# Kernel optimization log

Measured on AMD Instinct MI355X. Metric: run time of the kernel, lower is better.

The kernel has to match this reference:

```python
import jax, jax.numpy as jnp
import numpy as np

N = 2048
TEMP = 1.0


def _conv(x, w, b):
    y = jax.lax.conv_general_dilated(x, w, (1, 1), 'VALID',
                                     dimension_numbers=('NCHW', 'OIHW', 'NCHW'))
    return y + b[None, :, None, None]


def _pool(x):
    return jax.lax.reduce_window(x, -jnp.inf, jax.lax.max,
                                 (1, 1, 2, 2), (1, 1, 2, 2), 'VALID')


def setup_inputs() -> dict:
    key = jax.random.key(0)
    ks = jax.random.split(key, 20)
    s = 0.05
    idx = jnp.arange(N)
    positions = jnp.stack([idx // 64, idx % 64], axis=1).astype(jnp.int32)  # 32x64 grid
    return {
        'x': jax.random.normal(ks[0], (1, N, 1, 32, 32), jnp.float32),
        'positions': positions,
        'conv1_w': jax.random.normal(ks[1], (36, 1, 4, 4), jnp.float32) * s,
        'conv1_b': jnp.zeros((36,), jnp.float32),
        'conv2_w': jax.random.normal(ks[2], (48, 36, 3, 3), jnp.float32) * s,
        'conv2_b': jnp.zeros((48,), jnp.float32),
        'fc1_w': jax.random.normal(ks[3], (512, 1728), jnp.float32) * s,
        'fc1_b': jnp.zeros((512,), jnp.float32),
        'fc2_w': jax.random.normal(ks[4], (512, 512), jnp.float32) * s,
        'fc2_b': jnp.zeros((512,), jnp.float32),
        'nbr_w': jax.random.normal(ks[5], (512, 512), jnp.float32) * s,
        'nbr_b': jnp.zeros((512,), jnp.float32),
        'templates': jax.random.normal(ks[6], (10, 1024), jnp.float32),
        'proto_w': jax.random.normal(ks[7], (1024, 1024), jnp.float32) * s,
        'proto_b': jnp.zeros((1024,), jnp.float32),
        'glob_w1': jax.random.normal(ks[8], (128, 1024), jnp.float32) * s,
        'glob_b1': jnp.zeros((128,), jnp.float32),
        'glob_w2': jax.random.normal(ks[9], (1, 128), jnp.float32) * s,
        'glob_b2': jnp.zeros((1,), jnp.float32),
        'cls_w': jax.random.normal(ks[10], (2, 1024), jnp.float32) * s,
        'cls_b': jnp.zeros((2,), jnp.float32),
    }


def reference(x, positions, conv1_w, conv1_b, conv2_w, conv2_b,
              fc1_w, fc1_b, fc2_w, fc2_b, nbr_w, nbr_b,
              templates, proto_w, proto_b, glob_w1, glob_b1,
              glob_w2, glob_b2, cls_w, cls_b):
    xs = x[0]                                    # squeeze bag dim -> [N,1,32,32]
    h = _pool(jax.nn.relu(_conv(xs, conv1_w, conv1_b)))
    h = _pool(jax.nn.relu(_conv(h, conv2_w, conv2_b)))
    H = h.reshape(h.shape[0], -1)                # [N,1728]
    H = jax.nn.relu(H @ fc1_w.T + fc1_b)         # dropout is identity in eval
    H = jax.nn.relu(H @ fc2_w.T + fc2_b)         # [N,512]

    # --- neighbourhood attention (vectorized GAT-style gather/softmax) ---
    d = jnp.max(jnp.abs(positions[:, None, :] - positions[None, :, :]), axis=-1)
    mask = (d > 0) & (d <= 1)                    # [N,N] neighbor mask
    has = mask.any(axis=1)
    mask = jnp.where(has[:, None], mask, jnp.eye(mask.shape[0], dtype=bool))  # fallback: self
    An = jnp.tanh(H @ nbr_w.T + nbr_b)           # [N,512]
    logits = H @ An.T                            # logits[i,j] = tanh(W h_j) . h_i
    alphas = jax.nn.softmax(jnp.where(mask, logits, -jnp.inf), axis=1)
    Hn = alphas @ H                              # neighbourhood embeddings [N,512]
    H2 = jnp.concatenate([H, Hn], axis=1)        # [N,1024]

    # --- template (prototype) attention ---
    betas = jax.nn.softmax((jnp.tanh(H2 @ proto_w.T + proto_b) @ templates.T).T / TEMP, axis=1)  # [T,N]
    embs = betas @ H2                            # [T,1024]

    # --- global attention over templates ---
    g = jnp.tanh(embs @ glob_w1.T + glob_b1) @ glob_w2.T + glob_b2  # [T,1]
    gammas = jax.nn.softmax(g.T / TEMP, axis=1)  # [1,T]
    M = gammas @ embs                            # [1,1024]
    A = gammas @ betas                           # [1,N]
    Y_prob = jax.nn.sigmoid(M @ cls_w.T + cls_b) # [1,2]
    Y_hat = jnp.argmax(Y_prob, axis=1)
    return Y_prob, Y_hat, A
```

## Files before the change

kernel.cpp:

```cpp
#include <hip/hip_runtime.h>
#include <hip/hip_bf16.h>
#include <math.h>


typedef short short8 __attribute__((ext_vector_type(8)));
typedef float f32x4  __attribute__((ext_vector_type(4)));

__device__ inline short f2bf(float f) {
    unsigned u = __builtin_bit_cast(unsigned, f);
    u += 0x7fff + ((u >> 16) & 1);
    return (short)(u >> 16);
}
__device__ inline float bf2f(short h) {
    unsigned u = ((unsigned)(unsigned short)h) << 16;
    return __builtin_bit_cast(float, u);
}
__device__ inline f32x4 mfma16(short8 a, short8 b, f32x4 c) {
    return __builtin_amdgcn_mfma_f32_16x16x32_bf16(a, b, c, 0, 0, 0);
}
__device__ inline void splitstore(const float* s, short* hi, short* lo, int i) {
    float f = s[i];
    short h = f2bf(f);
    hi[i] = h;
    lo[i] = f2bf(f - bf2f(h));
}

__global__ __launch_bounds__(256) void prep_all_kernel(
    const float* __restrict__ fc1w, short* __restrict__ fc1whi, short* __restrict__ fc1wlo,
    const float* __restrict__ fc2w, short* __restrict__ fc2whi, short* __restrict__ fc2wlo,
    const float* __restrict__ nbrw, short* __restrict__ nbrwhi, short* __restrict__ nbrwlo,
    const float* __restrict__ prw,  short* __restrict__ prwhi,  short* __restrict__ prwlo,
    const float* __restrict__ w1,   short* __restrict__ w1m,
    const float* __restrict__ w2,   short* __restrict__ w2m,
    float* __restrict__ St, float* __restrict__ embs)
{
    const int b = blockIdx.x, tid = threadIdx.x;
    if (b < 3456) {
        int i = b*256 + tid; if (i < 884736) splitstore(fc1w, fc1whi, fc1wlo, i);
    } else if (b < 4480) {
        int i = (b-3456)*256 + tid; if (i < 262144) splitstore(fc2w, fc2whi, fc2wlo, i);
    } else if (b < 5504) {
        int i = (b-4480)*256 + tid; if (i < 262144) splitstore(nbrw, nbrwhi, nbrwlo, i);
    } else if (b < 9600) {
        int i = (b-5504)*256 + tid; if (i < 1048576) splitstore(prw, prwhi, prwlo, i);
    } else if (b < 9606) {
        int i = (b-9600)*256 + tid;
        if (i < 1536) {
            int c = i >> 5, k = i & 31;
            w1m[i] = (c < 36 && k < 16) ? f2bf(w1[c*16 + k]) : (short)0;
        }
    } else if (b < 9714) {
        int i = (b-9606)*256 + tid;
        if (i < 27648) {
            int oc = i / 576, r = i % 576, tap = r >> 6, c = r & 63;
            w2m[i] = (c < 36) ? f2bf(w2[oc*324 + c*9 + tap]) : (short)0;
        }
    } else if (b < 9794) {
        int i = (b-9714)*256 + tid; if (i < 20480) St[i] = 0.0f;
    } else {
        int i = (b-9794)*256 + tid; if (i < 10240) embs[i] = 0.0f;
    }
}

__global__ __launch_bounds__(64, 2) void conv_mfma_kernel(
    const float* __restrict__ x,
    const short* __restrict__ w1m,
    const float* __restrict__ b1,
    const short* __restrict__ w2m,
    const float* __restrict__ b2,
    short* __restrict__ Hfhi)
{
    __shared__ __align__(16) short sxb[2][1024];
    __shared__ __align__(16) short sh1[196*40 + 32];
    const int n = blockIdx.x, l = threadIdx.x;
    const int g = l >> 4, fr = l & 15;

    #pragma unroll
    for (int i = 0; i < 4; ++i) {
        const float4 v4 = ((const float4*)(x + (size_t)n*1024))[l + 64*i];
        short v[4] = { f2bf(v4.x), f2bf(v4.y), f2bf(v4.z), f2bf(v4.w) };
        const int c4 = (l + 64*i)*4;
        *(short4*)&sxb[0][c4] = *(short4*)v;
        if (c4 & 31) sxb[1][c4-1] = v[0];
        sxb[1][c4+0] = v[1];
        sxb[1][c4+1] = v[2];
        sxb[1][c4+2] = v[3];
    }
    if (l < 4) { short8 z = {}; *(short8*)&sh1[196*40 + l*8] = z; }
    short8 bw1[3];
    #pragma unroll
    for (int nt = 0; nt < 3; ++nt)
        bw1[nt] = *(const short8*)(w1m + (nt*16 + fr)*32 + g*8);
    __syncthreads();

    for (int mt = 0; mt < 49; ++mt) {
        const int pp = mt*16 + fr;
        const int q = pp >> 2, dd = pp & 3;
        const int iy0 = 2*(q/14) + (dd >> 1), ix0 = 2*(q%14) + (dd & 1);
        short8 af = {};
        if (g < 2) {
            const int par = ix0 & 1;
            const int colp = ix0 - par;
            const unsigned* p0 = (const unsigned*)&sxb[par][(iy0 + 2*g)*32 + colp];
            union { unsigned u[4]; short8 s; } uu;
            uu.u[0] = p0[0];  uu.u[1] = p0[1];
            uu.u[2] = p0[16]; uu.u[3] = p0[17];
            af = uu.s;
        }
        f32x4 acc[3] = {};
        #pragma unroll
        for (int nt = 0; nt < 3; ++nt) acc[nt] = mfma16(af, bw1[nt], acc[nt]);
        const int q1 = mt*4 + g;
        #pragma unroll
        for (int nt = 0; nt < 3; ++nt) {
            const int c = nt*16 + fr;
            if (c < 36) {
                float m = fmaxf(fmaxf(acc[nt][0], acc[nt][1]),
                                fmaxf(acc[nt][2], acc[nt][3]));
                m = fmaxf(m + b1[c], 0.0f);
                *(short*)((char*)sh1 + (q1*80 + c*2)) = f2bf(m);
            } else if (c < 40) {
                *(short*)((char*)sh1 + (q1*80 + c*2)) = 0;
            }
        }
    }
    __syncthreads();

    #pragma unroll
    for (int nt = 0; nt < 3; ++nt) {
        short8 bfr[18];
        {
            const short* wb = w2m + (size_t)(nt*16 + fr)*576 + g*8;
            #pragma unroll
            for (int ks = 0; ks < 18; ++ks)
                bfr[ks] = *(const short8*)(wb + ks*32);
        }
        for (int mt = 0; mt < 9; ++mt) {
            const int pp = mt*16 + fr;
            const int q2 = pp >> 2, dd = pp & 3;
            const int oy = 2*(q2/6) + (dd >> 1), ox = 2*(q2%6) + (dd & 1);
            f32x4 acc = {};
            #pragma unroll
            for (int ks = 0; ks < 18; ++ks) {
                const int tap = ks >> 1, half = ks & 1;
                const int hr = (oy + tap/3)*14 + ox + tap%3;
                const short8 a = *(const short8*)((char*)sh1 +
                    (hr*80 + half*64 + g*16));
                acc = mfma16(a, bfr[ks], acc);
            }
            const int oc = nt*16 + fr;
            float m = fmaxf(fmaxf(acc[0], acc[1]), fmaxf(acc[2], acc[3]));
            m = fmaxf(m + b2[oc], 0.0f);
            Hfhi[(size_t)n*1728 + oc*36 + (mt*4 + g)] = f2bf(m);
        }
    }
}

template<int ACT, int OUTF32, int OUTBF, int TSC>
__global__ __launch_bounds__(512, 2) void gemm_split_kernel(
    const short* __restrict__ Ahi,
    const short* __restrict__ Whi, const short* __restrict__ Wlo,
    const float* __restrict__ bias,
    float* __restrict__ Cf, short* __restrict__ Chi,
    const float* __restrict__ Tm, float* __restrict__ St,
    const int N, const int K)
{
    __shared__ __align__(16) short sA[4096];
    __shared__ __align__(16) short sB[2][4096];
    const int bn = blockIdx.x, bm = blockIdx.y;
    const int tid = threadIdx.x, l = tid & 63, w = tid >> 6, g = l >> 4, fr = l & 15;
    const int wm = w & 3, wn = w >> 2;
    const int srow = tid >> 3;
    const int wbyte = srow*128 + (tid & 7)*16;
    const int swb = (srow & 7) << 4;
    const size_t aoff = (size_t)(bm*64 + srow)*K + (tid & 7)*8;
    const size_t boff = (size_t)(bn*64 + srow)*K + (tid & 7)*8;
    f32x4 acc[2] = {};
    short8 ra = *(const short8*)(Ahi + aoff);
    short8 rb0 = *(const short8*)(Whi + boff);
    short8 rb1 = *(const short8*)(Wlo + boff);
    for (int k0 = 0; k0 < K; k0 += 64) {
        __syncthreads();
        *(short8*)((char*)sA       + (wbyte ^ swb)) = ra;
        *(short8*)((char*)&sB[0][0] + (wbyte ^ swb)) = rb0;
        *(short8*)((char*)&sB[1][0] + (wbyte ^ swb)) = rb1;
        __syncthreads();
        if (k0 + 64 < K) {
            ra  = *(const short8*)(Ahi + aoff + k0 + 64);
            rb0 = *(const short8*)(Whi + boff + k0 + 64);
            rb1 = *(const short8*)(Wlo + boff + k0 + 64);
        }
        const int ar = wm*16 + fr, asw = (ar & 7) << 4;
        const short8 ah0 = *(const short8*)((char*)sA + ((ar*128      + g*16) ^ asw));
        const short8 ah1 = *(const short8*)((char*)sA + ((ar*128 + 64 + g*16) ^ asw));
        #pragma unroll
        for (int ntl = 0; ntl < 2; ++ntl) {
            const int br = (wn*2 + ntl)*16 + fr, bsw = (br & 7) << 4;
            const short8 bh0 = *(const short8*)((char*)&sB[0][0] + ((br*128      + g*16) ^ bsw));
            const short8 bh1 = *(const short8*)((char*)&sB[0][0] + ((br*128 + 64 + g*16) ^ bsw));
            const short8 bl0 = *(const short8*)((char*)&sB[1][0] + ((br*128      + g*16) ^ bsw));
            const short8 bl1 = *(const short8*)((char*)&sB[1][0] + ((br*128 + 64 + g*16) ^ bsw));
            acc[ntl] = mfma16(ah0, bh0, acc[ntl]);
            acc[ntl] = mfma16(ah1, bh1, acc[ntl]);
            acc[ntl] = mfma16(ah0, bl0, acc[ntl]);
            acc[ntl] = mfma16(ah1, bl1, acc[ntl]);
        }
    }
    float pv[2][4];
    #pragma unroll
    for (int ntl = 0; ntl < 2; ++ntl) {
        const int col = bn*64 + (wn*2 + ntl)*16 + fr;
        const float bv = bias[col];
        #pragma unroll
        for (int i = 0; i < 4; ++i) {
            const int row = bm*64 + wm*16 + g*4 + i;
            float v = acc[ntl][i] + bv;
            if (ACT == 1) v = fmaxf(v, 0.0f);
            if (ACT == 2) v = tanhf(v);
            pv[ntl][i] = v;
            const size_t idx = (size_t)row*N + col;
            if (OUTF32) Cf[idx] = v;
            if (OUTBF)  Chi[idx] = f2bf(v);
        }
    }
    if (TSC) {
        for (int t = 0; t < 10; ++t) {
            float tm[2];
            #pragma unroll
            for (int ntl = 0; ntl < 2; ++ntl)
                tm[ntl] = Tm[t*1024 + bn*64 + (wn*2 + ntl)*16 + fr];
            float part[4];
            #pragma unroll
            for (int i = 0; i < 4; ++i) {
                float s = 0.0f;
                #pragma unroll
                for (int ntl = 0; ntl < 2; ++ntl) s = fmaf(pv[ntl][i], tm[ntl], s);
                #pragma unroll
                for (int m = 1; m <= 8; m <<= 1) s += __shfl_xor(s, m);
                part[i] = s;
            }
            if (fr == 0) {
                #pragma unroll
                for (int i = 0; i < 4; ++i)
                    atomicAdd(&St[t*2048 + bm*64 + wm*16 + g*4 + i], part[i]);
            }
        }
    }
}

__global__ __launch_bounds__(64) void nbr_attn_kernel(
    const float* __restrict__ H, const float* __restrict__ An,
    short* __restrict__ H2hi)
{
    const int i = blockIdx.x;
    const int lane = threadIdx.x;
    const int r = i >> 6, c = i & 63;
    const int DR[8] = {-1,-1,-1, 0, 0, 1, 1, 1};
    const int DC[8] = {-1, 0, 1,-1, 1,-1, 0, 1};
    int nbr[8]; bool val[8];
    #pragma unroll
    for (int j = 0; j < 8; ++j) {
        const int rr = r + DR[j], cc = c + DC[j];
        val[j] = (rr >= 0 && rr < 32 && cc >= 0 && cc < 64);
        nbr[j] = val[j] ? rr*64 + cc : i;
    }
    float hi[8];
    #pragma unroll
    for (int q = 0; q < 8; ++q) hi[q] = H[(size_t)i*512 + q*64 + lane];
    float av[8][8];
    #pragma unroll
    for (int j = 0; j < 8; ++j) {
        const float* an = An + (size_t)nbr[j]*512 + lane;
        #pragma unroll
        for (int q = 0; q < 8; ++q) av[j][q] = an[q*64];
    }
    float lg[8];
    #pragma unroll
    for (int j = 0; j < 8; ++j) {
        float s = 0.0f;
        #pragma unroll
        for (int q = 0; q < 8; ++q) s = fmaf(hi[q], av[j][q], s);
        #pragma unroll
        for (int off = 32; off; off >>= 1) s += __shfl_xor(s, off);
        lg[j] = val[j] ? s : -1e30f;
    }
    float mx = -1e30f;
    #pragma unroll
    for (int j = 0; j < 8; ++j) mx = fmaxf(mx, lg[j]);
    float sum = 0.0f; float al[8];
    #pragma unroll
    for (int j = 0; j < 8; ++j) { al[j] = expf(lg[j]-mx); sum += al[j]; }
    const float inv = 1.0f/sum;
    #pragma unroll
    for (int j = 0; j < 8; ++j) {
        const float* hj = H + (size_t)nbr[j]*512 + lane;
        #pragma unroll
        for (int q = 0; q < 8; ++q) av[j][q] = hj[q*64];
    }
    float hn[8] = {};
    #pragma unroll
    for (int j = 0; j < 8; ++j) {
        const float a = al[j]*inv;
        #pragma unroll
        for (int q = 0; q < 8; ++q) hn[q] = fmaf(a, av[j][q], hn[q]);
    }
    #pragma unroll
    for (int q = 0; q < 8; ++q) {
        const size_t i0 = (size_t)i*1024 + q*64 + lane;
        H2hi[i0]       = f2bf(hi[q]);
        H2hi[i0 + 512] = f2bf(hn[q]);
    }
}

__global__ __launch_bounds__(256) void beta_embs_kernel(
    const float* __restrict__ St,
    const short* __restrict__ H2hi,
    float* __restrict__ embs,
    float* __restrict__ minv)
{
    const int t = blockIdx.y;
    const int tid = threadIdx.x;
    __shared__ float red[256];
    __shared__ float sb[256];
    float mx = -1e30f;
    for (int n = tid; n < 2048; n += 256) mx = fmaxf(mx, St[t*2048+n]);
    red[tid] = mx; __syncthreads();
    for (int s = 128; s; s >>= 1) { if (tid < s) red[tid] = fmaxf(red[tid], red[tid+s]); __syncthreads(); }
    mx = red[0]; __syncthreads();
    float sum = 0.0f;
    for (int n = tid; n < 2048; n += 256) sum += expf(St[t*2048+n]-mx);
    red[tid] = sum; __syncthreads();
    for (int s = 128; s; s >>= 1) { if (tid < s) red[tid] += red[tid+s]; __syncthreads(); }
    const float inv = 1.0f/red[0];
    if (blockIdx.x == 0 && tid == 0) { minv[t*2+0] = mx; minv[t*2+1] = inv; }
    const int colc = blockIdx.x & 3;
    const int nc   = blockIdx.x >> 2;
    sb[tid] = expf(St[t*2048 + nc*256 + tid] - mx) * inv;
    __syncthreads();
    const int col = colc*256 + tid;
    float acc = 0.0f;
    for (int j = 0; j < 256; ++j)
        acc = fmaf(sb[j], bf2f(H2hi[(size_t)(nc*256+j)*1024 + col]), acc);
    atomicAdd(&embs[t*1024+col], acc);
}

__global__ __launch_bounds__(64) void glob_g2_kernel(
    const float* __restrict__ embs, const float* __restrict__ gw1,
    const float* __restrict__ gb1, const float* __restrict__ gw2,
    float* __restrict__ gpart)
{
    const int k = blockIdx.x, t = blockIdx.y, lane = threadIdx.x;
    const float* e  = embs + t*1024 + lane;
    const float* wv = gw1 + k*1024 + lane;
    float s = 0.0f;
    #pragma unroll
    for (int q = 0; q < 16; ++q) s = fmaf(e[q*64], wv[q*64], s);
    #pragma unroll
    for (int off = 32; off; off >>= 1) s += __shfl_xor(s, off);
    if (lane == 0) gpart[t*128 + k] = tanhf(s + gb1[k]) * gw2[k];
}

__global__ __launch_bounds__(256) void final3_kernel(
    const float* __restrict__ gpart, const float* __restrict__ gb2,
    const float* __restrict__ embs,  const float* __restrict__ St,
    const float* __restrict__ minv,
    const float* __restrict__ cw, const float* __restrict__ cb,
    float* __restrict__ out)
{
    __shared__ float gam[10];
    __shared__ float sM[1024];
    __shared__ float red[256];
    __shared__ float gv[10];
    __shared__ float smx[10], sinv[10];
    __shared__ float v0s;
    const int tid = threadIdx.x;
    for (int t = 0; t < 10; ++t) {
        float s = (tid < 128) ? gpart[t*128 + tid] : 0.0f;
        red[tid] = s; __syncthreads();
        for (int st = 128; st; st >>= 1) { if (tid < st) red[tid] += red[tid+st]; __syncthreads(); }
        if (tid == 0) gv[t] = red[0];
        __syncthreads();
    }
    if (tid < 10) { smx[tid] = minv[tid*2]; sinv[tid] = minv[tid*2+1]; }
    if (tid == 0) {
        float mx = -1e30f;
        for (int t = 0; t < 10; ++t) mx = fmaxf(mx, gv[t] + gb2[0]);
        float sum = 0.0f;
        for (int t = 0; t < 10; ++t) { gam[t] = expf(gv[t] + gb2[0] - mx); sum += gam[t]; }
        for (int t = 0; t < 10; ++t) gam[t] /= sum;
    }
    __syncthreads();
    for (int col = tid; col < 1024; col += 256) {
        float m = 0.0f;
        for (int t = 0; t < 10; ++t) m = fmaf(gam[t], embs[t*1024+col], m);
        sM[col] = m;
    }
    for (int n = tid; n < 2048; n += 256) {
        float a = 0.0f;
        for (int t = 0; t < 10; ++t)
            a = fmaf(gam[t], expf(St[t*2048+n]-smx[t])*sinv[t], a);
        out[3+n] = a;
    }
    __syncthreads();
    float s0 = 0.0f, s1 = 0.0f;
    for (int q = tid; q < 1024; q += 256) {
        s0 = fmaf(sM[q], cw[q], s0);
        s1 = fmaf(sM[q], cw[1024+q], s1);
    }
    red[tid] = s0; __syncthreads();
    for (int s = 128; s; s >>= 1) { if (tid < s) red[tid] += red[tid+s]; __syncthreads(); }
    if (tid == 0) v0s = red[0];
    __syncthreads();
    red[tid] = s1; __syncthreads();
    for (int s = 128; s; s >>= 1) { if (tid < s) red[tid] += red[tid+s]; __syncthreads(); }
    if (tid == 0) {
        const float l0 = v0s + cb[0], l1 = red[0] + cb[1];
        const float p0 = 1.0f/(1.0f+expf(-l0));
        const float p1 = 1.0f/(1.0f+expf(-l1));
        out[0] = p0; out[1] = p1;
        out[2] = (p1 > p0) ? 1.0f : 0.0f;
    }
}

extern "C" void kernel_launch(void* const* d_in, const int* in_sizes, int n_in,
                              void* d_out, int out_size, void* d_ws, size_t ws_size,
                              hipStream_t stream)
{
    (void)in_sizes; (void)n_in; (void)out_size; (void)ws_size;
    const float* x        = (const float*)d_in[0];
    const float* conv1_w  = (const float*)d_in[2];
    const float* conv1_b  = (const float*)d_in[3];
    const float* conv2_w  = (const float*)d_in[4];
    const float* conv2_b  = (const float*)d_in[5];
    const float* fc1_w    = (const float*)d_in[6];
    const float* fc1_b    = (const float*)d_in[7];
    const float* fc2_w    = (const float*)d_in[8];
    const float* fc2_b    = (const float*)d_in[9];
    const float* nbr_w    = (const float*)d_in[10];
    const float* nbr_b    = (const float*)d_in[11];
    const float* templ    = (const float*)d_in[12];
    const float* proto_w  = (const float*)d_in[13];
    const float* proto_b  = (const float*)d_in[14];
    const float* glob_w1  = (const float*)d_in[15];
    const float* glob_b1  = (const float*)d_in[16];
    const float* glob_w2  = (const float*)d_in[17];
    const float* glob_b2  = (const float*)d_in[18];
    const float* cls_w    = (const float*)d_in[19];
    const float* cls_b    = (const float*)d_in[20];
    float* out = (float*)d_out;

    char* p = (char*)d_ws;
    auto alloc = [&](size_t bytes) { char* r = p; p += (bytes + 255) & ~(size_t)255; return r; };
    short* Hfhi   = (short*)alloc((size_t)2048*1728*2);
    short* Hfc1hi = (short*)alloc((size_t)2048*512*2);
    float* H      = (float*)alloc((size_t)2048*512*4);
    short* Hhi    = (short*)alloc((size_t)2048*512*2);
    float* An     = (float*)alloc((size_t)2048*512*4);
    short* H2hi   = (short*)alloc((size_t)2048*1024*2);
    float* St     = (float*)alloc((size_t)10*2048*4);
    float* minv   = (float*)alloc(10*2*4);
    float* embs   = (float*)alloc((size_t)10*1024*4);
    float* gpart  = (float*)alloc((size_t)10*128*4);
    short* w1m    = (short*)alloc(1536*2);
    short* w2m    = (short*)alloc(27648*2);
    short* fc1whi = (short*)alloc((size_t)512*1728*2);
    short* fc1wlo = (short*)alloc((size_t)512*1728*2);
    short* fc2whi = (short*)alloc((size_t)512*512*2);
    short* fc2wlo = (short*)alloc((size_t)512*512*2);
    short* nbrwhi = (short*)alloc((size_t)512*512*2);
    short* nbrwlo = (short*)alloc((size_t)512*512*2);
    short* prwhi  = (short*)alloc((size_t)1024*1024*2);
    short* prwlo  = (short*)alloc((size_t)1024*1024*2);

    prep_all_kernel<<<9834, 256, 0, stream>>>(
        fc1_w, fc1whi, fc1wlo, fc2_w, fc2whi, fc2wlo,
        nbr_w, nbrwhi, nbrwlo, proto_w, prwhi, prwlo,
        conv1_w, w1m, conv2_w, w2m, St, embs);

    conv_mfma_kernel<<<2048, 64, 0, stream>>>(x, w1m, conv1_b, w2m, conv2_b, Hfhi);
    gemm_split_kernel<1,0,1,0><<<dim3(8,32), 512, 0, stream>>>(
        Hfhi, fc1whi, fc1wlo, fc1_b, nullptr, Hfc1hi, nullptr, nullptr, 512, 1728);
    gemm_split_kernel<1,1,1,0><<<dim3(8,32), 512, 0, stream>>>(
        Hfc1hi, fc2whi, fc2wlo, fc2_b, H, Hhi, nullptr, nullptr, 512, 512);
    gemm_split_kernel<2,1,0,0><<<dim3(8,32), 512, 0, stream>>>(
        Hhi, nbrwhi, nbrwlo, nbr_b, An, nullptr, nullptr, nullptr, 512, 512);
    nbr_attn_kernel<<<2048, 64, 0, stream>>>(H, An, H2hi);
    gemm_split_kernel<2,0,0,1><<<dim3(16,32), 512, 0, stream>>>(
        H2hi, prwhi, prwlo, proto_b, nullptr, nullptr, templ, St, 1024, 1024);
    beta_embs_kernel<<<dim3(32,10), 256, 0, stream>>>(St, H2hi, embs, minv);
    glob_g2_kernel<<<dim3(128,10), 64, 0, stream>>>(embs, glob_w1, glob_b1, glob_w2, gpart);
    final3_kernel<<<1, 256, 0, stream>>>(gpart, glob_b2, embs, St, minv, cls_w, cls_b, out);
}
```

Before: 161.5 us.

## Pack conv2 weights to drop channel padding and reuse A fragments across output tiles

Conv2's im2col K dimension drops from 18 padded k-steps (64 channels per tap, 36 real) to 11 packed k-steps. The leftover 4 channels of each tap are gathered into two extra fragments. The loop order is swapped so each A-fragment set is loaded once per M tile and reused across all three output-channel tiles, with all B fragments preloaded into registers. This cuts MFMA count and LDS reads, but raises register pressure (33 short8 B fragments plus 11 A fragments), which may reduce occupancy or cause spills under the 64x2 launch bounds.

```diff
diff --git a/kernel.cpp b/kernel.cpp
--- a/kernel.cpp
+++ b/kernel.cpp
@@ -31,7 +31,7 @@
     const float* __restrict__ nbrw, short* __restrict__ nbrwhi, short* __restrict__ nbrwlo,
     const float* __restrict__ prw,  short* __restrict__ prwhi,  short* __restrict__ prwlo,
     const float* __restrict__ w1,   short* __restrict__ w1m,
-    const float* __restrict__ w2,   short* __restrict__ w2m,
+    const float* __restrict__ w2,   short* __restrict__ w2mp,
     float* __restrict__ St, float* __restrict__ embs)
 {
     const int b = blockIdx.x, tid = threadIdx.x;
@@ -49,16 +49,20 @@
             int c = i >> 5, k = i & 31;
             w1m[i] = (c < 36 && k < 16) ? f2bf(w1[c*16 + k]) : (short)0;
         }
-    } else if (b < 9714) {
+    } else if (b < 9672) {
         int i = (b-9606)*256 + tid;
-        if (i < 27648) {
-            int oc = i / 576, r = i % 576, tap = r >> 6, c = r & 63;
-            w2m[i] = (c < 36) ? f2bf(w2[oc*324 + c*9 + tap]) : (short)0;
-        }
-    } else if (b < 9794) {
-        int i = (b-9714)*256 + tid; if (i < 20480) St[i] = 0.0f;
+        if (i < 16896) {
+            int oc = i / 352, r = i % 352, ks = r >> 5, j = r & 31;
+            float v = 0.0f;
+            if (ks < 9)          v = w2[oc*324 + j*9 + ks];
+            else if (ks == 9)    v = w2[oc*324 + (32 + (j & 3))*9 + (j >> 2)];
+            else if (j < 4)      v = w2[oc*324 + (32 + j)*9 + 8];
+            w2mp[i] = f2bf(v);
+        }
+    } else if (b < 9752) {
+        int i = (b-9672)*256 + tid; if (i < 20480) St[i] = 0.0f;
     } else {
-        int i = (b-9794)*256 + tid; if (i < 10240) embs[i] = 0.0f;
+        int i = (b-9752)*256 + tid; if (i < 10240) embs[i] = 0.0f;
     }
 }
 
@@ -66,12 +70,12 @@
     const float* __restrict__ x,
     const short* __restrict__ w1m,
     const float* __restrict__ b1,
-    const short* __restrict__ w2m,
+    const short* __restrict__ w2mp,
     const float* __restrict__ b2,
     short* __restrict__ Hfhi)
 {
     __shared__ __align__(16) short sxb[2][1024];
-    __shared__ __align__(16) short sh1[196*40 + 32];
+    __shared__ __align__(16) short sh1[196*40];
     const int n = blockIdx.x, l = threadIdx.x;
     const int g = l >> 4, fr = l & 15;
 
@@ -86,11 +90,18 @@
         sxb[1][c4+1] = v[2];
         sxb[1][c4+2] = v[3];
     }
-    if (l < 4) { short8 z = {}; *(short8*)&sh1[196*40 + l*8] = z; }
     short8 bw1[3];
     #pragma unroll
     for (int nt = 0; nt < 3; ++nt)
         bw1[nt] = *(const short8*)(w1m + (nt*16 + fr)*32 + g*8);
+    short8 bfr[3][11];
+    #pragma unroll
+    for (int nt = 0; nt < 3; ++nt) {
+        const short* wb = w2mp + (size_t)(nt*16 + fr)*352 + g*8;
+        #pragma unroll
+        for (int ks = 0; ks < 11; ++ks)
+            bfr[nt][ks] = *(const short8*)(wb + ks*32);
+    }
     __syncthreads();
 
     for (int mt = 0; mt < 49; ++mt) {
@@ -119,35 +130,44 @@
                                 fmaxf(acc[nt][2], acc[nt][3]));
                 m = fmaxf(m + b1[c], 0.0f);
                 *(short*)((char*)sh1 + (q1*80 + c*2)) = f2bf(m);
-            } else if (c < 40) {
-                *(short*)((char*)sh1 + (q1*80 + c*2)) = 0;
             }
         }
     }
     __syncthreads();
 
-    #pragma unroll
-    for (int nt = 0; nt < 3; ++nt) {
-        short8 bfr[18];
+    for (int mt = 0; mt < 9; ++mt) {
+        const int pp = mt*16 + fr;
+        const int q2 = pp >> 2, dd = pp & 3;
+        const int oy = 2*(q2/6) + (dd >> 1), ox = 2*(q2%6) + (dd & 1);
+        short8 av[11];
+        #pragma unroll
+        for (int tap = 0; tap < 9; ++tap) {
+            const int hr = (oy + tap/3)*14 + ox + tap%3;
+            av[tap] = *(const short8*)((char*)sh1 + (hr*80 + g*16));
+        }
         {
-            const short* wb = w2m + (size_t)(nt*16 + fr)*576 + g*8;
-            #pragma unroll
-            for (int ks = 0; ks < 18; ++ks)
-                bfr[ks] = *(const short8*)(wb + ks*32);
-        }
-        for (int mt = 0; mt < 9; ++mt) {
-            const int pp = mt*16 + fr;
-            const int q2 = pp >> 2, dd = pp & 3;
-            const int oy = 2*(q2/6) + (dd >> 1), ox = 2*(q2%6) + (dd & 1);
+            const int t0 = g*2, t1 = g*2 + 1;
+            const int h0 = (oy + t0/3)*14 + ox + t0%3;
+            const int h1 = (oy + t1/3)*14 + ox + t1%3;
+            union { short4 h[2]; short8 s; } u9;
+            u9.h[0] = *(const short4*)((char*)sh1 + (h0*80 + 64));
+            u9.h[1] = *(const short4*)((char*)sh1 + (h1*80 + 64));
+            av[9] = u9.s;
+        }
+        {
+            short8 a10 = {};
+            if (g == 0) {
+                const int h8 = (oy + 2)*14 + ox + 2;
+                *(short4*)&a10 = *(const short4*)((char*)sh1 + (h8*80 + 64));
+            }
+            av[10] = a10;
+        }
+        #pragma unroll
+        for (int nt = 0; nt < 3; ++nt) {
             f32x4 acc = {};
             #pragma unroll
-            for (int ks = 0; ks < 18; ++ks) {
-                const int tap = ks >> 1, half = ks & 1;
-                const int hr = (oy + tap/3)*14 + ox + tap%3;
-                const short8 a = *(const short8*)((char*)sh1 +
-                    (hr*80 + half*64 + g*16));
-                acc = mfma16(a, bfr[ks], acc);
-            }
+            for (int ks = 0; ks < 11; ++ks)
+                acc = mfma16(av[ks], bfr[nt][ks], acc);
             const int oc = nt*16 + fr;
             float m = fmaxf(fmaxf(acc[0], acc[1]), fmaxf(acc[2], acc[3]));
             m = fmaxf(m + b2[oc], 0.0f);
@@ -462,7 +482,7 @@
     float* embs   = (float*)alloc((size_t)10*1024*4);
     float* gpart  = (float*)alloc((size_t)10*128*4);
     short* w1m    = (short*)alloc(1536*2);
-    short* w2m    = (short*)alloc(27648*2);
+    short* w2mp   = (short*)alloc(16896*2);
     short* fc1whi = (short*)alloc((size_t)512*1728*2);
     short* fc1wlo = (short*)alloc((size_t)512*1728*2);
     short* fc2whi = (short*)alloc((size_t)512*512*2);
@@ -472,12 +492,12 @@
     short* prwhi  = (short*)alloc((size_t)1024*1024*2);
     short* prwlo  = (short*)alloc((size_t)1024*1024*2);
 
-    prep_all_kernel<<<9834, 256, 0, stream>>>(
+    prep_all_kernel<<<9792, 256, 0, stream>>>(
         fc1_w, fc1whi, fc1wlo, fc2_w, fc2whi, fc2wlo,
         nbr_w, nbrwhi, nbrwlo, proto_w, prwhi, prwlo,
-        conv1_w, w1m, conv2_w, w2m, St, embs);
-
-    conv_mfma_kernel<<<2048, 64, 0, stream>>>(x, w1m, conv1_b, w2m, conv2_b, Hfhi);
+        conv1_w, w1m, conv2_w, w2mp, St, embs);
+
+    conv_mfma_kernel<<<2048, 64, 0, stream>>>(x, w1m, conv1_b, w2mp, conv2_b, Hfhi);
     gemm_split_kernel<1,0,1,0><<<dim3(8,32), 512, 0, stream>>>(
         Hfhi, fc1whi, fc1wlo, fc1_b, nullptr, Hfc1hi, nullptr, nullptr, 512, 1728);
     gemm_split_kernel<1,1,1,0><<<dim3(8,32), 512, 0, stream>>>(
```

Result: faster. 145.5 us (-9.9%).
